# Performance work log

Measured on AMD Instinct MI355X. Metric: run time of the kernel, lower is better.

Reference implementation:

```python
import jax, jax.numpy as jnp
import numpy as np

B, S, D = 2, 2048, 1024
H, DH = 16, 64  # n_heads, d_head; inner_dim = H*DH = 1024


def setup_inputs() -> dict:
    key = jax.random.key(0)
    ks = jax.random.split(key, 6)
    s = 0.02
    return {
        "query": jax.random.normal(ks[0], (B, S, D), jnp.float32),
        "context": jax.random.normal(ks[1], (B, S, D), jnp.float32),
        "Wq": jax.random.normal(ks[2], (D, H * DH), jnp.float32) * s,
        "Wk": jax.random.normal(ks[3], (D, H * DH), jnp.float32) * s,
        "Wv": jax.random.normal(ks[4], (D, H * DH), jnp.float32) * s,
        "Wo": jax.random.normal(ks[5], (H * DH, D), jnp.float32) * s,
        "bo": jnp.zeros((D,), jnp.float32),
    }


def reference(query, context, Wq, Wk, Wv, Wo, bo):
    scale = DH ** -0.5
    # projections -> [B, H, S, DH]
    q = (query @ Wq).reshape(B, S, H, DH).transpose(0, 2, 1, 3)
    k = (context @ Wk).reshape(B, S, H, DH).transpose(0, 2, 1, 3)
    v = (context @ Wv).reshape(B, S, H, DH).transpose(0, 2, 1, 3)
    scores = jnp.einsum("bhqd,bhkd->bhqk", q, k) * scale  # [B,H,S,S]
    probs = jax.nn.softmax(scores, axis=-1)
    out = jnp.einsum("bhqk,bhkd->bhqd", probs, v)  # [B,H,S,DH]
    out = out.transpose(0, 2, 1, 3).reshape(B, S, H * DH)
    return out @ Wo + bo
```

## Files before the change

kernel.cpp:

```cpp
#include <hip/hip_runtime.h>
#include <hip/hip_bf16.h>

typedef __attribute__((ext_vector_type(8))) short bf16x8;
typedef __attribute__((ext_vector_type(4))) float f32x4;
typedef __attribute__((ext_vector_type(16))) float f32x16;

#define B_ 2
#define S_ 2048
#define D_ 1024
#define H_ 16

__device__ __forceinline__ unsigned short f2bf(float x) {
  unsigned u = __float_as_uint(x);
  unsigned r = (u + 0x7fffu + ((u >> 16) & 1u)) >> 16;
  return (unsigned short)r;
}

__device__ __forceinline__ unsigned cvt_pk_bf16(float lo, float hi) {
  unsigned r;
  asm("v_cvt_pk_bf16_f32 %0, %1, %2" : "=v"(r) : "v"(lo), "v"(hi));
  return r;
}

__device__ __forceinline__ void gload_lds16(const void* g, void* l) {
  __builtin_amdgcn_global_load_lds((const __attribute__((address_space(1))) void*)g,
                                   (__attribute__((address_space(3))) void*)l, 16, 0, 0);
}

#define VM_BARRIER(N) do {                                   \
    asm volatile("s_waitcnt vmcnt(" #N ")" ::: "memory");    \
    __builtin_amdgcn_s_barrier();                            \
    __builtin_amdgcn_sched_barrier(0);                       \
  } while (0)

__global__ __launch_bounds__(256) void prep_kernel(const float* __restrict__ query,
                                                   const float* __restrict__ ctx,
                                                   const float* __restrict__ Wq, const float* __restrict__ Wk,
                                                   const float* __restrict__ Wv, const float* __restrict__ Wo,
                                                   unsigned short* __restrict__ qb, unsigned short* __restrict__ cb,
                                                   unsigned short* __restrict__ WqT, unsigned short* __restrict__ WkT,
                                                   unsigned short* __restrict__ WvT, unsigned short* __restrict__ WoT) {
  __shared__ float tile[32][33];
  int bid = blockIdx.x;
  if (bid < 8192) {
    const float* s = bid < 4096 ? query : ctx;
    unsigned short* d = bid < 4096 ? qb : cb;
    int i = (bid & 4095) * 256 + threadIdx.x;
    float4 v = ((const float4*)s)[i];
    ushort4 o;
    o.x = f2bf(v.x); o.y = f2bf(v.y); o.z = f2bf(v.z); o.w = f2bf(v.w);
    ((ushort4*)d)[i] = o;
    return;
  }
  int tid = bid - 8192;
  int z = tid >> 10, r = tid & 1023;
  const float* W; unsigned short* WT;
  if (z == 0)      { W = Wq; WT = WqT; }
  else if (z == 1) { W = Wk; WT = WkT; }
  else if (z == 2) { W = Wv; WT = WvT; }
  else             { W = Wo; WT = WoT; }
  int r0 = (r >> 5) * 32, c0 = (r & 31) * 32;
  int t = threadIdx.x;
  int lr = t >> 3, lc = (t & 7) * 4;
  float4 v = *(const float4*)&W[(size_t)(r0 + lr) * 1024 + c0 + lc];
  tile[lr][lc + 0] = v.x; tile[lr][lc + 1] = v.y; tile[lr][lc + 2] = v.z; tile[lr][lc + 3] = v.w;
  __syncthreads();
  ushort4 o;
  o.x = f2bf(tile[lc + 0][lr]);
  o.y = f2bf(tile[lc + 1][lr]);
  o.z = f2bf(tile[lc + 2][lr]);
  o.w = f2bf(tile[lc + 3][lr]);
  *(ushort4*)&WT[(size_t)(c0 + lr) * 1024 + r0 + lc] = o;
}

__device__ __forceinline__ void gemm_core(const unsigned short* __restrict__ A,
                                          const unsigned short* __restrict__ BT,
                                          int m0, int n0,
                                          unsigned short* As, unsigned short* Bs,
                                          f32x4 (&acc)[4][4]) {
  const int t = threadIdx.x, w = t >> 6, l = t & 63;
  const int lr = l & 15, lg = (l >> 4) * 8;
  const int wm = (w >> 1) * 64, wn = (w & 1) * 64;
  const int K = 1024;

#define GSTAGE(buf, k0) do {                                                               \
    _Pragma("unroll")                                                                      \
    for (int it_ = 0; it_ < 2; ++it_) {                                                    \
      int o_ = t * 16 + it_ * 4096;                                                        \
      int row_ = o_ >> 6, ce_ = (o_ & 63) >> 1;                                            \
      gload_lds16(A + (size_t)(m0 + row_) * K + (k0) + ce_,                                \
                  (char*)As + (buf) * 8192 + it_ * 4096 + w * 1024);                       \
      gload_lds16(BT + (size_t)(n0 + row_) * K + (k0) + ce_,                               \
                  (char*)Bs + (buf) * 8192 + it_ * 4096 + w * 1024);                       \
    }                                                                                      \
  } while (0)

  GSTAGE(0, 0);
  GSTAGE(1, 32);
  VM_BARRIER(4);
  int cur = 0;
  for (int kt = 0; kt < 32; ++kt) {
    int nb = cur + 2; if (nb >= 3) nb -= 3;
    if (kt < 30) GSTAGE(nb, (kt + 2) * 32);
    bf16x8 af[4], bfr[4];
#pragma unroll
    for (int mi = 0; mi < 4; ++mi) af[mi] = *(const bf16x8*)&As[cur * 4096 + (wm + mi * 16 + lr) * 32 + lg];
#pragma unroll
    for (int ni = 0; ni < 4; ++ni) bfr[ni] = *(const bf16x8*)&Bs[cur * 4096 + (wn + ni * 16 + lr) * 32 + lg];
    __builtin_amdgcn_s_setprio(1);
#pragma unroll
    for (int mi = 0; mi < 4; ++mi)
#pragma unroll
      for (int ni = 0; ni < 4; ++ni)
        acc[mi][ni] = __builtin_amdgcn_mfma_f32_16x16x32_bf16(af[mi], bfr[ni], acc[mi][ni], 0, 0, 0);
    __builtin_amdgcn_s_setprio(0);
    if (kt < 30) VM_BARRIER(4);
    else if (kt == 30) VM_BARRIER(0);
    cur = (cur == 2) ? 0 : cur + 1;
  }
#undef GSTAGE
}

__global__ __launch_bounds__(256) void gemm_qkv(const unsigned short* __restrict__ qb,
                                                const unsigned short* __restrict__ cb,
                                                const unsigned short* __restrict__ WqT,
                                                const unsigned short* __restrict__ WkT,
                                                const unsigned short* __restrict__ WvT,
                                                unsigned short* __restrict__ qp,
                                                unsigned short* __restrict__ kp,
                                                unsigned short* __restrict__ vt) {
  __shared__ unsigned short As[3 * 4096];
  __shared__ unsigned short Bs[3 * 4096];
  int wg = (blockIdx.x & 7) * 96 + (blockIdx.x >> 3);
  int z = wg >> 8, r = wg & 255;
  const unsigned short *A, *BT; unsigned short* C; int N, bx, by;
  float osc;
  if (z == 0)      { A = qb;  BT = WqT; C = qp; N = 1024; bx = r & 31; by = r >> 5; osc = 0.125f * 1.44269504089f; }
  else if (z == 1) { A = cb;  BT = WkT; C = kp; N = 1024; bx = r & 31; by = r >> 5; osc = 1.f; }
  else             { A = WvT; BT = cb;  C = vt; N = 4096; bx = r & 7;  by = r >> 3; osc = 1.f; }
  f32x4 acc[4][4];
#pragma unroll
  for (int mi = 0; mi < 4; ++mi)
#pragma unroll
    for (int ni = 0; ni < 4; ++ni) acc[mi][ni] = {0.f, 0.f, 0.f, 0.f};
  gemm_core(A, BT, bx * 128, by * 128, As, Bs, acc);
  const int t = threadIdx.x, w = t >> 6, l = t & 63;
  const int lr = l & 15, lg4 = (l >> 4) * 4;
  const int wm = (w >> 1) * 64, wn = (w & 1) * 64;
#pragma unroll
  for (int mi = 0; mi < 4; ++mi)
#pragma unroll
    for (int ni = 0; ni < 4; ++ni)
#pragma unroll
      for (int j = 0; j < 4; ++j)
        C[(size_t)(bx * 128 + wm + mi * 16 + lg4 + j) * N + by * 128 + wn + ni * 16 + lr] =
            f2bf(acc[mi][ni][j] * osc);
}

__global__ __launch_bounds__(256) void gemm_out(const unsigned short* __restrict__ A,
                                                const unsigned short* __restrict__ BT,
                                                const float* __restrict__ bias,
                                                float* __restrict__ C) {
  __shared__ unsigned short As[3 * 4096];
  __shared__ unsigned short Bs[3 * 4096];
  int wg = (blockIdx.x & 7) * 32 + (blockIdx.x >> 3);
  int bx = wg & 31, by = wg >> 5;
  f32x4 acc[4][4];
#pragma unroll
  for (int mi = 0; mi < 4; ++mi)
#pragma unroll
    for (int ni = 0; ni < 4; ++ni) acc[mi][ni] = {0.f, 0.f, 0.f, 0.f};
  gemm_core(A, BT, bx * 128, by * 128, As, Bs, acc);
  const int t = threadIdx.x, w = t >> 6, l = t & 63;
  const int lr = l & 15, lg4 = (l >> 4) * 4;
  const int wm = (w >> 1) * 64, wn = (w & 1) * 64;
#pragma unroll
  for (int mi = 0; mi < 4; ++mi)
#pragma unroll
    for (int ni = 0; ni < 4; ++ni) {
      int col = by * 128 + wn + ni * 16 + lr;
      float bv = bias[col];
#pragma unroll
      for (int j = 0; j < 4; ++j)
        C[(size_t)(bx * 128 + wm + mi * 16 + lg4 + j) * 1024 + col] = acc[mi][ni][j] + bv;
    }
}

__global__ __launch_bounds__(256) void attn_kernel(const unsigned short* __restrict__ Q,
                                                   const unsigned short* __restrict__ Kp,
                                                   const unsigned short* __restrict__ Vt,
                                                   unsigned short* __restrict__ O) {
  __shared__ char lds[49152];
  const int t = threadIdx.x, w = t >> 6, l = t & 63;
  const int l31 = l & 31, hi = l >> 5;
  const int nf = (blockIdx.x & 7) * 64 + (blockIdx.x >> 3);
  const int qt = nf & 15, h = (nf >> 4) & 15, b = nf >> 8;

  const int q = qt * 128 + w * 32 + l31;
  const size_t qbase = ((size_t)(b * S_ + q)) * 1024 + h * 64;
  bf16x8 qf[4];
#pragma unroll
  for (int c = 0; c < 4; ++c) qf[c] = *(const bf16x8*)&Q[qbase + c * 16 + hi * 8];

  const size_t kbase = (size_t)b * S_ * 1024 + h * 64;
  const size_t vtb = (size_t)(h * 64) * 4096 + (size_t)b * 2048;

  f32x16 oaccA[2], oaccB[2];
#pragma unroll
  for (int d = 0; d < 2; ++d)
#pragma unroll
    for (int r = 0; r < 16; ++r) { oaccA[d][r] = 0.f; oaccB[d][r] = 0.f; }
  float l_run = 0.f;

#define STAGE(bsel, kv0) do {                                                          \
    char* kdst = lds + (bsel) * 16384;                                                 \
    char* vdst = kdst + 8192;                                                          \
    _Pragma("unroll")                                                                  \
    for (int it_ = 0; it_ < 2; ++it_) {                                                \
      const int off_ = it_ * 4096 + w * 1024 + l * 16;                                 \
      const int row_ = off_ >> 7, cb_ = off_ & 127;                                    \
      const int sc_ = (cb_ ^ ((row_ & 7) << 4)) >> 1;                                  \
      gload_lds16(Kp + kbase + (size_t)((kv0) + row_) * 1024 + sc_,                    \
                  kdst + it_ * 4096 + w * 1024);                                       \
      gload_lds16(Vt + vtb + (size_t)row_ * 4096 + (kv0) + sc_,                        \
                  vdst + it_ * 4096 + w * 1024);                                       \
    }                                                                                  \
  } while (0)

  STAGE(0, 0);
  STAGE(1, 64);
  VM_BARRIER(4);
  int cur = 0;
  const int sw = (l & 7) << 4;

  for (int tile = 0; tile < 32; ++tile) {
    int nb = cur + 2; if (nb >= 3) nb -= 3;
    if (tile < 30) STAGE(nb, (tile + 2) * 64);
    const char* kb = lds + cur * 16384;
    const char* vb = kb + 8192;

    f32x16 sacc[2];
#pragma unroll
    for (int kvb = 0; kvb < 2; ++kvb) {
#pragma unroll
      for (int r = 0; r < 16; ++r) sacc[kvb][r] = 0.f;
      const int row = kvb * 32 + l31;
      __builtin_amdgcn_s_setprio(1);
#pragma unroll
      for (int c = 0; c < 4; ++c) {
        bf16x8 kf = *(const bf16x8*)(kb + row * 128 + ((c * 32 + hi * 16) ^ sw));
        sacc[kvb] = __builtin_amdgcn_mfma_f32_32x32x16_bf16(kf, qf[c], sacc[kvb], 0, 0, 0);
      }
      __builtin_amdgcn_s_setprio(0);
    }

    float rs = 0.f;
#pragma unroll
    for (int kvb = 0; kvb < 2; ++kvb)
#pragma unroll
      for (int r = 0; r < 16; ++r) {
        float p = exp2f(sacc[kvb][r]);
        sacc[kvb][r] = p;
        rs += p;
      }
    rs += __shfl_xor(rs, 32, 64);
    l_run += rs;

#pragma unroll
    for (int c = 0; c < 4; ++c) {
      const int sb = c >> 1, r0 = (c & 1) * 8;
      unsigned wA = cvt_pk_bf16(sacc[sb][r0 + 0], sacc[sb][r0 + 1]);
      unsigned wB = cvt_pk_bf16(sacc[sb][r0 + 2], sacc[sb][r0 + 3]);
      unsigned wC = cvt_pk_bf16(sacc[sb][r0 + 4], sacc[sb][r0 + 5]);
      unsigned wD = cvt_pk_bf16(sacc[sb][r0 + 6], sacc[sb][r0 + 7]);
      unsigned s0 = hi ? wA : wC;
      unsigned s1 = hi ? wB : wD;
      unsigned x0 = (unsigned)__shfl_xor((int)s0, 32, 64);
      unsigned x1 = (unsigned)__shfl_xor((int)s1, 32, 64);
      union { unsigned u[4]; bf16x8 v; } pf;
      pf.u[0] = hi ? x0 : wA;
      pf.u[1] = hi ? x1 : wB;
      pf.u[2] = hi ? wC : x0;
      pf.u[3] = hi ? wD : x1;
      __builtin_amdgcn_s_setprio(1);
#pragma unroll
      for (int d = 0; d < 2; ++d) {
        const int vrow = d * 32 + l31;
        bf16x8 vf = *(const bf16x8*)(vb + vrow * 128 + ((c * 32 + hi * 16) ^ sw));
        if (c & 1) oaccB[d] = __builtin_amdgcn_mfma_f32_32x32x16_bf16(vf, pf.v, oaccB[d], 0, 0, 0);
        else       oaccA[d] = __builtin_amdgcn_mfma_f32_32x32x16_bf16(vf, pf.v, oaccA[d], 0, 0, 0);
      }
      __builtin_amdgcn_s_setprio(0);
    }
    if (tile < 30) VM_BARRIER(4);
    else if (tile == 30) VM_BARRIER(0);
    cur = (cur == 2) ? 0 : cur + 1;
  }

  const float inv = 1.f / l_run;
#pragma unroll
  for (int d = 0; d < 2; ++d)
#pragma unroll
    for (int rg = 0; rg < 4; ++rg) {
      ushort4 o4;
      o4.x = f2bf((oaccA[d][rg * 4 + 0] + oaccB[d][rg * 4 + 0]) * inv);
      o4.y = f2bf((oaccA[d][rg * 4 + 1] + oaccB[d][rg * 4 + 1]) * inv);
      o4.z = f2bf((oaccA[d][rg * 4 + 2] + oaccB[d][rg * 4 + 2]) * inv);
      o4.w = f2bf((oaccA[d][rg * 4 + 3] + oaccB[d][rg * 4 + 3]) * inv);
      *(ushort4*)&O[qbase + d * 32 + rg * 8 + hi * 4] = o4;
    }
#undef STAGE
}

extern "C" void kernel_launch(void* const* d_in, const int* in_sizes, int n_in,
                              void* d_out, int out_size, void* d_ws, size_t ws_size,
                              hipStream_t stream) {
  const float* query   = (const float*)d_in[0];
  const float* context = (const float*)d_in[1];
  const float* Wq = (const float*)d_in[2];
  const float* Wk = (const float*)d_in[3];
  const float* Wv = (const float*)d_in[4];
  const float* Wo = (const float*)d_in[5];
  const float* bo = (const float*)d_in[6];
  float* out = (float*)d_out;

  const size_t NA = (size_t)B_ * S_ * D_;
  const size_t NW = (size_t)D_ * D_;
  unsigned short* ws  = (unsigned short*)d_ws;
  unsigned short* qb  = ws;
  unsigned short* cb  = qb + NA;
  unsigned short* WqT = cb + NA;
  unsigned short* WkT = WqT + NW;
  unsigned short* WvT = WkT + NW;
  unsigned short* WoT = WvT + NW;
  unsigned short* qp  = WoT + NW;
  unsigned short* kp  = qp + NA;
  unsigned short* vt  = kp + NA;
  unsigned short* ao  = qb;

  prep_kernel<<<12288, 256, 0, stream>>>(query, context, Wq, Wk, Wv, Wo,
                                         qb, cb, WqT, WkT, WvT, WoT);
  gemm_qkv<<<768, 256, 0, stream>>>(qb, cb, WqT, WkT, WvT, qp, kp, vt);
  attn_kernel<<<512, 256, 0, stream>>>(qp, kp, vt, ao);
  gemm_out<<<256, 256, 0, stream>>>(ao, WoT, bo, out);
}
```

Before: 146.6 us.

## Split attention over two KV halves with a combine pass; shrink output GEMM tiles

The attention kernel now splits each (batch, head, query-tile) over two halves of the key/value sequence. This doubles the grid to 1024 workgroups and cuts LDS to a double buffer. Each half writes an unnormalized bf16 partial output plus its row sum, and a new combine kernel adds the halves and normalizes. The output GEMM is templated to 128x64 tiles, giving 512 workgroups instead of 256 so the CUs are better filled. The cost is an extra kernel launch, extra global traffic for the partials, extra bf16 rounding of the partials, and a shorter prefetch pipeline in attention.

```diff
diff --git a/kernel.cpp b/kernel.cpp
--- a/kernel.cpp
+++ b/kernel.cpp
@@ -14,6 +14,10 @@
   unsigned u = __float_as_uint(x);
   unsigned r = (u + 0x7fffu + ((u >> 16) & 1u)) >> 16;
   return (unsigned short)r;
+}
+
+__device__ __forceinline__ float bf2f(unsigned short x) {
+  return __uint_as_float((unsigned)x << 16);
 }
 
 __device__ __forceinline__ unsigned cvt_pk_bf16(float lo, float hi) {
@@ -73,48 +77,57 @@
   *(ushort4*)&WT[(size_t)(c0 + lr) * 1024 + r0 + lc] = o;
 }
 
+template<int BM, int BN>
 __device__ __forceinline__ void gemm_core(const unsigned short* __restrict__ A,
                                           const unsigned short* __restrict__ BT,
                                           int m0, int n0,
                                           unsigned short* As, unsigned short* Bs,
-                                          f32x4 (&acc)[4][4]) {
+                                          f32x4 (&acc)[BM / 32][BN / 32]) {
   const int t = threadIdx.x, w = t >> 6, l = t & 63;
   const int lr = l & 15, lg = (l >> 4) * 8;
-  const int wm = (w >> 1) * 64, wn = (w & 1) * 64;
-  const int K = 1024;
+  const int wm = (w >> 1) * (BM / 2), wn = (w & 1) * (BN / 2);
+  constexpr int K = 1024;
+  constexpr int AI = BM / 64, BI = BN / 64, NLD = AI + BI;
 
 #define GSTAGE(buf, k0) do {                                                               \
     _Pragma("unroll")                                                                      \
-    for (int it_ = 0; it_ < 2; ++it_) {                                                    \
+    for (int it_ = 0; it_ < AI; ++it_) {                                                   \
       int o_ = t * 16 + it_ * 4096;                                                        \
       int row_ = o_ >> 6, ce_ = (o_ & 63) >> 1;                                            \
       gload_lds16(A + (size_t)(m0 + row_) * K + (k0) + ce_,                                \
-                  (char*)As + (buf) * 8192 + it_ * 4096 + w * 1024);                       \
+                  (char*)As + (buf) * (BM * 64) + it_ * 4096 + w * 1024);                  \
+    }                                                                                      \
+    _Pragma("unroll")                                                                      \
+    for (int it_ = 0; it_ < BI; ++it_) {                                                   \
+      int o_ = t * 16 + it_ * 4096;                                                        \
+      int row_ = o_ >> 6, ce_ = (o_ & 63) >> 1;                                            \
       gload_lds16(BT + (size_t)(n0 + row_) * K + (k0) + ce_,                               \
-                  (char*)Bs + (buf) * 8192 + it_ * 4096 + w * 1024);                       \
+                  (char*)Bs + (buf) * (BN * 64) + it_ * 4096 + w * 1024);                  \
     }                                                                                      \
   } while (0)
 
   GSTAGE(0, 0);
   GSTAGE(1, 32);
-  VM_BARRIER(4);
+  if constexpr (NLD == 4) VM_BARRIER(4); else VM_BARRIER(3);
   int cur = 0;
   for (int kt = 0; kt < 32; ++kt) {
     int nb = cur + 2; if (nb >= 3) nb -= 3;
     if (kt < 30) GSTAGE(nb, (kt + 2) * 32);
-    bf16x8 af[4], bfr[4];
-#pragma unroll
-    for (int mi = 0; mi < 4; ++mi) af[mi] = *(const bf16x8*)&As[cur * 4096 + (wm + mi * 16 + lr) * 32 + lg];
-#pragma unroll
-    for (int ni = 0; ni < 4; ++ni) bfr[ni] = *(const bf16x8*)&Bs[cur * 4096 + (wn + ni * 16 + lr) * 32 + lg];
+    bf16x8 af[BM / 32], bfr[BN / 32];
+#pragma unroll
+    for (int mi = 0; mi < BM / 32; ++mi)
+      af[mi] = *(const bf16x8*)&As[cur * (BM * 32) + (wm + mi * 16 + lr) * 32 + lg];
+#pragma unroll
+    for (int ni = 0; ni < BN / 32; ++ni)
+      bfr[ni] = *(const bf16x8*)&Bs[cur * (BN * 32) + (wn + ni * 16 + lr) * 32 + lg];
     __builtin_amdgcn_s_setprio(1);
 #pragma unroll
-    for (int mi = 0; mi < 4; ++mi)
-#pragma unroll
-      for (int ni = 0; ni < 4; ++ni)
+    for (int mi = 0; mi < BM / 32; ++mi)
+#pragma unroll
+      for (int ni = 0; ni < BN / 32; ++ni)
         acc[mi][ni] = __builtin_amdgcn_mfma_f32_16x16x32_bf16(af[mi], bfr[ni], acc[mi][ni], 0, 0, 0);
     __builtin_amdgcn_s_setprio(0);
-    if (kt < 30) VM_BARRIER(4);
+    if (kt < 30) { if constexpr (NLD == 4) VM_BARRIER(4); else VM_BARRIER(3); }
     else if (kt == 30) VM_BARRIER(0);
     cur = (cur == 2) ? 0 : cur + 1;
   }
@@ -143,7 +156,7 @@
   for (int mi = 0; mi < 4; ++mi)
 #pragma unroll
     for (int ni = 0; ni < 4; ++ni) acc[mi][ni] = {0.f, 0.f, 0.f, 0.f};
-  gemm_core(A, BT, bx * 128, by * 128, As, Bs, acc);
+  gemm_core<128, 128>(A, BT, bx * 128, by * 128, As, Bs, acc);
   const int t = threadIdx.x, w = t >> 6, l = t & 63;
   const int lr = l & 15, lg4 = (l >> 4) * 4;
   const int wm = (w >> 1) * 64, wn = (w & 1) * 64;
@@ -162,23 +175,23 @@
                                                 const float* __restrict__ bias,
                                                 float* __restrict__ C) {
   __shared__ unsigned short As[3 * 4096];
-  __shared__ unsigned short Bs[3 * 4096];
-  int wg = (blockIdx.x & 7) * 32 + (blockIdx.x >> 3);
-  int bx = wg & 31, by = wg >> 5;
-  f32x4 acc[4][4];
+  __shared__ unsigned short Bs[3 * 2048];
+  int wg = (blockIdx.x & 7) * 64 + (blockIdx.x >> 3);
+  int by = wg & 15, bx = wg >> 4;
+  f32x4 acc[4][2];
 #pragma unroll
   for (int mi = 0; mi < 4; ++mi)
 #pragma unroll
-    for (int ni = 0; ni < 4; ++ni) acc[mi][ni] = {0.f, 0.f, 0.f, 0.f};
-  gemm_core(A, BT, bx * 128, by * 128, As, Bs, acc);
+    for (int ni = 0; ni < 2; ++ni) acc[mi][ni] = {0.f, 0.f, 0.f, 0.f};
+  gemm_core<128, 64>(A, BT, bx * 128, by * 64, As, Bs, acc);
   const int t = threadIdx.x, w = t >> 6, l = t & 63;
   const int lr = l & 15, lg4 = (l >> 4) * 4;
-  const int wm = (w >> 1) * 64, wn = (w & 1) * 64;
+  const int wm = (w >> 1) * 64, wn = (w & 1) * 32;
 #pragma unroll
   for (int mi = 0; mi < 4; ++mi)
 #pragma unroll
-    for (int ni = 0; ni < 4; ++ni) {
-      int col = by * 128 + wn + ni * 16 + lr;
+    for (int ni = 0; ni < 2; ++ni) {
+      int col = by * 64 + wn + ni * 16 + lr;
       float bv = bias[col];
 #pragma unroll
       for (int j = 0; j < 4; ++j)
@@ -189,11 +202,14 @@
 __global__ __launch_bounds__(256) void attn_kernel(const unsigned short* __restrict__ Q,
                                                    const unsigned short* __restrict__ Kp,
                                                    const unsigned short* __restrict__ Vt,
-                                                   unsigned short* __restrict__ O) {
-  __shared__ char lds[49152];
+                                                   unsigned short* __restrict__ Op0,
+                                                   unsigned short* __restrict__ Op1,
+                                                   float* __restrict__ Lp) {
+  __shared__ char lds[32768];
   const int t = threadIdx.x, w = t >> 6, l = t & 63;
   const int l31 = l & 31, hi = l >> 5;
-  const int nf = (blockIdx.x & 7) * 64 + (blockIdx.x >> 3);
+  const int u = (blockIdx.x & 7) * 128 + (blockIdx.x >> 3);
+  const int half = u >> 9, nf = u & 511;
   const int qt = nf & 15, h = (nf >> 4) & 15, b = nf >> 8;
 
   const int q = qt * 128 + w * 32 + l31;
@@ -202,8 +218,8 @@
 #pragma unroll
   for (int c = 0; c < 4; ++c) qf[c] = *(const bf16x8*)&Q[qbase + c * 16 + hi * 8];
 
-  const size_t kbase = (size_t)b * S_ * 1024 + h * 64;
-  const size_t vtb = (size_t)(h * 64) * 4096 + (size_t)b * 2048;
+  const size_t kbase = (size_t)b * S_ * 1024 + h * 64 + ((size_t)half << 20);
+  const size_t vtb = (size_t)(h * 64) * 4096 + (size_t)b * 2048 + half * 1024;
 
   f32x16 oaccA[2], oaccB[2];
 #pragma unroll
@@ -228,14 +244,12 @@
   } while (0)
 
   STAGE(0, 0);
-  STAGE(1, 64);
-  VM_BARRIER(4);
+  VM_BARRIER(0);
   int cur = 0;
   const int sw = (l & 7) << 4;
 
-  for (int tile = 0; tile < 32; ++tile) {
-    int nb = cur + 2; if (nb >= 3) nb -= 3;
-    if (tile < 30) STAGE(nb, (tile + 2) * 64);
+  for (int tile = 0; tile < 16; ++tile) {
+    if (tile < 15) STAGE(cur ^ 1, (tile + 1) * 64);
     const char* kb = lds + cur * 16384;
     const char* vb = kb + 8192;
 
@@ -292,24 +306,49 @@
       }
       __builtin_amdgcn_s_setprio(0);
     }
-    if (tile < 30) VM_BARRIER(4);
-    else if (tile == 30) VM_BARRIER(0);
-    cur = (cur == 2) ? 0 : cur + 1;
+    if (tile < 15) VM_BARRIER(0);
+    cur ^= 1;
   }
 
-  const float inv = 1.f / l_run;
+  unsigned short* Op = half ? Op1 : Op0;
 #pragma unroll
   for (int d = 0; d < 2; ++d)
 #pragma unroll
     for (int rg = 0; rg < 4; ++rg) {
       ushort4 o4;
-      o4.x = f2bf((oaccA[d][rg * 4 + 0] + oaccB[d][rg * 4 + 0]) * inv);
-      o4.y = f2bf((oaccA[d][rg * 4 + 1] + oaccB[d][rg * 4 + 1]) * inv);
-      o4.z = f2bf((oaccA[d][rg * 4 + 2] + oaccB[d][rg * 4 + 2]) * inv);
-      o4.w = f2bf((oaccA[d][rg * 4 + 3] + oaccB[d][rg * 4 + 3]) * inv);
-      *(ushort4*)&O[qbase + d * 32 + rg * 8 + hi * 4] = o4;
+      o4.x = f2bf(oaccA[d][rg * 4 + 0] + oaccB[d][rg * 4 + 0]);
+      o4.y = f2bf(oaccA[d][rg * 4 + 1] + oaccB[d][rg * 4 + 1]);
+      o4.z = f2bf(oaccA[d][rg * 4 + 2] + oaccB[d][rg * 4 + 2]);
+      o4.w = f2bf(oaccA[d][rg * 4 + 3] + oaccB[d][rg * 4 + 3]);
+      *(ushort4*)&Op[qbase + d * 32 + rg * 8 + hi * 4] = o4;
     }
+  if (!hi) Lp[half * 65536 + (b * 16 + h) * 2048 + q] = l_run;
 #undef STAGE
+}
+
+__global__ __launch_bounds__(256) void combine_kernel(unsigned short* __restrict__ Op0,
+                                                      const unsigned short* __restrict__ Op1,
+                                                      const float* __restrict__ Lp) {
+  int e8 = blockIdx.x * 256 + threadIdx.x;
+  int r = e8 >> 7, c = (e8 & 127) * 8;
+  int b = r >> 11, s = r & 2047, h = c >> 6;
+  float la = Lp[(b * 16 + h) * 2048 + s];
+  float lb = Lp[65536 + (b * 16 + h) * 2048 + s];
+  float inv = 1.f / (la + lb);
+  size_t off = (size_t)r * 1024 + c;
+  ushort4 a0 = *(ushort4*)&Op0[off], a1 = *(ushort4*)&Op0[off + 4];
+  ushort4 b0 = *(const ushort4*)&Op1[off], b1 = *(const ushort4*)&Op1[off + 4];
+  ushort4 o0, o1;
+  o0.x = f2bf((bf2f(a0.x) + bf2f(b0.x)) * inv);
+  o0.y = f2bf((bf2f(a0.y) + bf2f(b0.y)) * inv);
+  o0.z = f2bf((bf2f(a0.z) + bf2f(b0.z)) * inv);
+  o0.w = f2bf((bf2f(a0.w) + bf2f(b0.w)) * inv);
+  o1.x = f2bf((bf2f(a1.x) + bf2f(b1.x)) * inv);
+  o1.y = f2bf((bf2f(a1.y) + bf2f(b1.y)) * inv);
+  o1.z = f2bf((bf2f(a1.z) + bf2f(b1.z)) * inv);
+  o1.w = f2bf((bf2f(a1.w) + bf2f(b1.w)) * inv);
+  *(ushort4*)&Op0[off] = o0;
+  *(ushort4*)&Op0[off + 4] = o1;
 }
 
 extern "C" void kernel_launch(void* const* d_in, const int* in_sizes, int n_in,
@@ -336,11 +375,15 @@
   unsigned short* qp  = WoT + NW;
   unsigned short* kp  = qp + NA;
   unsigned short* vt  = kp + NA;
+  unsigned short* Op0 = qb;
+  unsigned short* Op1 = cb;
+  float* Lp = (float*)WqT;
   unsigned short* ao  = qb;
 
   prep_kernel<<<12288, 256, 0, stream>>>(query, context, Wq, Wk, Wv, Wo,
                                          qb, cb, WqT, WkT, WvT, WoT);
   gemm_qkv<<<768, 256, 0, stream>>>(qb, cb, WqT, WkT, WvT, qp, kp, vt);
-  attn_kernel<<<512, 256, 0, stream>>>(qp, kp, vt, ao);
-  gemm_out<<<256, 256, 0, stream>>>(ao, WoT, bo, out);
-}
+  attn_kernel<<<1024, 256, 0, stream>>>(qp, kp, vt, Op0, Op1, Lp);
+  combine_kernel<<<2048, 256, 0, stream>>>(Op0, Op1, Lp);
+  gemm_out<<<512, 256, 0, stream>>>(ao, WoT, bo, out);
+}
```

New measurement: 150.2 us. 1.02x slower.
